# Optimization experiments

Hardware: AMD Instinct MI355X
Metric: run time of the kernel (lower is better)

## Reference

```python
import jax, jax.numpy as jnp
import numpy as np

BSZ, S, F, K, PI = 32, 4096, 512, 4, 1


def setup_inputs() -> dict:
    key = jax.random.key(0)
    ks = jax.random.split(key, 5)
    x = jax.random.normal(ks[0], (BSZ, S, F), dtype=jnp.float32)
    s = 1.0 / np.float32(np.sqrt(F))
    Wu = jax.random.normal(ks[1], (F, F), dtype=jnp.float32) * s
    P = jax.random.normal(ks[2], (F // K, F), dtype=jnp.float32) * s
    Q = jax.random.normal(ks[3], (F, PI * F), dtype=jnp.float32) * s
    Bb = jax.random.normal(ks[4], (F // K, PI * F), dtype=jnp.float32) * 0.01
    return {"x": x, "Wu": Wu, "P": P, "Q": Q, "Bb": Bb}


def reference(x, Wu, P, Q, Bb):
    # x: [B, S, F]
    B_, S_, F_ = x.shape
    Fk = P.shape[0]          # F // k
    k = F_ // Fk
    piF = Q.shape[1]
    # Ux = relu(x @ Wu): [B, S, F]
    Ux = jax.nn.relu(jnp.einsum('bsf,fg->bsg', x, Wu))
    # KMaxPooling over sequence axis: transpose to [B, F, S], top_k -> [B, F, k]
    topv = jax.lax.top_k(jnp.transpose(Ux, (0, 2, 1)), k)[0]
    # original does a raw reshape [B, F, k] -> [B, k, F] (element order preserved)
    z = topv.reshape(B_, k, F_)
    # P is reshaped in call() from [F/k, F] to [F, F/k]
    P2 = P.reshape(F_, Fk)
    # diag(z_i) @ P2 == z_i[:, None] * P2 -> [B, k, F, F/k], then per-i reshape to [B, F/k, F]
    zp = (z[:, :, :, None] * P2[None, None, :, :]).reshape(B_, k, Fk, F_)
    # @ Q, bias add, relu: [B, k, F/k, pi*F]
    out = jax.nn.relu(jnp.einsum('bkmf,fq->bkmq', zp, Q) + Bb[None, None, :, :])
    # concat over k along axis 1 -> [B, F, pi*F]
    return out.reshape(B_, F_, piF)
```

## Files before the change

### kernel.cpp

```cpp
#include <hip/hip_runtime.h>

#define BSZ   32
#define SEQ   4096
#define FDIM  512
#define KTOP  4
#define FK    128
#define MTOT  (BSZ * SEQ)
#define NCHUNK 32

#define BM2  256
#define BN2  256
#define BK2  64
#define NKT  (FDIM / BK2)

typedef __attribute__((ext_vector_type(8))) short bf16x8;
typedef __attribute__((ext_vector_type(4))) float f32x4;
typedef __attribute__((ext_vector_type(8))) unsigned short u16x8;

typedef __attribute__((address_space(1))) void void_g;
typedef __attribute__((address_space(3))) void void_l;

static __device__ __forceinline__ void load_lds16(const void* g, void* l) {
  __builtin_amdgcn_global_load_lds((void_g*)g, (void_l*)l, 16, 0, 0);
}

static __device__ __forceinline__ unsigned short f2bf(float f) {
  unsigned int u = __float_as_uint(f);
  unsigned int r = (u + 0x7fffu + ((u >> 16) & 1u)) >> 16;
  return (unsigned short)r;
}

static __device__ __forceinline__ void sort2(float& a, float& b) {
  float mx = fmaxf(a, b), mn = fminf(a, b); a = mx; b = mn;
}
static __device__ __forceinline__ void sort4(float& a, float& b, float& c, float& d) {
  sort2(a, b); sort2(c, d); sort2(a, c); sort2(b, d); sort2(b, c);
}
static __device__ __forceinline__ void merge4(float& a, float& b, float& c, float& d,
                                              float e, float f, float g, float h) {
  float m0 = fmaxf(a, h), m1 = fmaxf(b, g), m2 = fmaxf(c, f), m3 = fmaxf(d, e);
  sort2(m0, m2); sort2(m1, m3); sort2(m0, m1); sort2(m2, m3);
  a = m0; b = m1; c = m2; d = m3;
}

__global__ __launch_bounds__(256) void cvt_wuT_kernel(const float* __restrict__ Wu,
                                                      unsigned short* __restrict__ WuT) {
  int nn = blockIdx.x;
  for (int k = threadIdx.x; k < FDIM; k += blockDim.x)
    WuT[(size_t)nn * FDIM + k] = f2bf(Wu[(size_t)k * FDIM + nn]);
}

__global__ __launch_bounds__(256) void compute_R_kernel(const float* __restrict__ P,
                                                        const float* __restrict__ Q,
                                                        float* __restrict__ R) {
  int g = blockIdx.y;
  int q = blockIdx.x * 256 + threadIdx.x;
  __shared__ float p2[FK];
  if (threadIdx.x < FK) p2[threadIdx.x] = P[(size_t)g * FK + threadIdx.x];
  __syncthreads();
  const float* Qb = Q + (size_t)((g & 3) * FK) * FDIM + q;
  float s = 0.f;
#pragma unroll 8
  for (int m = 0; m < FK; ++m) s = fmaf(p2[m], Qb[(size_t)m * FDIM], s);
  R[(size_t)g * FDIM + q] = s;
}

__global__ __launch_bounds__(512, 1) void gemm_topk_kernel(
    const float* __restrict__ X, const unsigned short* __restrict__ Bt,
    float* __restrict__ cand) {
  __shared__ __align__(16) unsigned short As[2][BM2 * BK2];
  __shared__ __align__(16) unsigned short Bs[2][BM2 * BK2];

  const int tid = threadIdx.x;
  const int lane = tid & 63;
  const int w = tid >> 6;
  const int wm = w & 1, wn = w >> 1;

  const int xcd = blockIdx.x & 7;
  const int jj = blockIdx.x >> 3;
  const int t = xcd * 128 + jj;
  const int mtile = t >> 1, ntile = t & 1;
  const int m0 = mtile * BM2, n0 = ntile * BN2;

  const int arow = tid >> 3;
  const int asc = tid & 7;
  const int aswz = (arow & 7) << 4;
  const float* axp[4];
  int aldst[4];
#pragma unroll
  for (int i = 0; i < 4; ++i) {
    const int row = i * 64 + arow;
    axp[i] = X + (size_t)(m0 + row) * FDIM + asc * 8;
    aldst[i] = row * 128 + ((asc * 16) ^ aswz);
  }
  float4 arA[4][2];

#define ALOADS(kt)                                                             \
  {                                                                            \
    _Pragma("unroll") for (int i = 0; i < 4; ++i) {                            \
      const float4* p = (const float4*)(axp[i] + (kt) * BK2);                  \
      arA[i][0] = p[0];                                                        \
      arA[i][1] = p[1];                                                        \
    }                                                                          \
  }

#define AWRITES(buf)                                                           \
  {                                                                            \
    _Pragma("unroll") for (int i = 0; i < 4; ++i) {                            \
      u16x8 o;                                                                 \
      o[0] = f2bf(arA[i][0].x); o[1] = f2bf(arA[i][0].y);                      \
      o[2] = f2bf(arA[i][0].z); o[3] = f2bf(arA[i][0].w);                      \
      o[4] = f2bf(arA[i][1].x); o[5] = f2bf(arA[i][1].y);                      \
      o[6] = f2bf(arA[i][1].z); o[7] = f2bf(arA[i][1].w);                      \
      *(u16x8*)((char*)As[buf] + aldst[i]) = o;                                \
    }                                                                          \
  }

  const char* bsrc[4];
#pragma unroll
  for (int i = 0; i < 4; ++i) {
    int o = i * 8192 + tid * 16;
    int row = o >> 7;
    int colb = (o & 127) ^ ((row & 7) << 4);
    bsrc[i] = (const char*)(Bt + (size_t)(n0 + row) * FDIM) + colb;
  }
  const int ldst = (tid >> 6) * 512;

#define STAGE_B(kt, buf)                                                       \
  {                                                                            \
    _Pragma("unroll") for (int i = 0; i < 4; ++i)                              \
        load_lds16(bsrc[i] + (kt) * 128, (void*)(&Bs[buf][i * 4096 + ldst]));  \
  }

  const int lr = lane & 15;
  const int g16 = lane >> 4;
  const int swz = (lr & 7) << 4;
  const int arow0 = (wm * 128 + lr) * 128;
  const int brow0 = (wn * 64 + lr) * 128;

  f32x4 acc[8][4];
#pragma unroll
  for (int mi = 0; mi < 8; ++mi)
#pragma unroll
    for (int ni = 0; ni < 4; ++ni) acc[mi][ni] = {0.f, 0.f, 0.f, 0.f};

#define PHASE(Ap, Bp, mh, nh, ...)                                             \
  {                                                                            \
    bf16x8 af[4][2], bfr[2][2];                                                \
    _Pragma("unroll") for (int j = 0; j < 4; ++j)                              \
        _Pragma("unroll") for (int kq = 0; kq < 2; ++kq)                       \
            af[j][kq] = *(const bf16x8*)((Ap) + arow0 + ((mh)*4 + j) * 2048 +  \
                                         ((kq * 64 + g16 * 16) ^ swz));        \
    _Pragma("unroll") for (int j = 0; j < 2; ++j)                              \
        _Pragma("unroll") for (int kq = 0; kq < 2; ++kq)                       \
            bfr[j][kq] = *(const bf16x8*)((Bp) + brow0 + ((nh)*2 + j) * 2048 + \
                                          ((kq * 64 + g16 * 16) ^ swz));       \
    __VA_ARGS__;                                                               \
    __builtin_amdgcn_s_barrier();                                              \
    __builtin_amdgcn_s_setprio(1);                                             \
    _Pragma("unroll") for (int j = 0; j < 4; ++j)                              \
        _Pragma("unroll") for (int jn = 0; jn < 2; ++jn)                       \
            _Pragma("unroll") for (int kq = 0; kq < 2; ++kq)                   \
                acc[(mh)*4 + j][(nh)*2 + jn] =                                 \
                    __builtin_amdgcn_mfma_f32_16x16x32_bf16(                   \
                        af[j][kq], bfr[jn][kq], acc[(mh)*4 + j][(nh)*2 + jn],  \
                        0, 0, 0);                                              \
    __builtin_amdgcn_s_setprio(0);                                             \
  }

  ALOADS(0);
  AWRITES(0);
  STAGE_B(0, 0);
  asm volatile("s_waitcnt vmcnt(0) lgkmcnt(0)" ::: "memory");
  __builtin_amdgcn_s_barrier();
  __builtin_amdgcn_sched_barrier(0);

#pragma unroll 1
  for (int kt = 0; kt < NKT; ++kt) {
    const int c = kt & 1;
    const char* Ap = (const char*)As[c];
    const char* Bp = (const char*)Bs[c];
    const int last = (kt == NKT - 1);

    PHASE(Ap, Bp, 0, 0, if (!last) ALOADS(kt + 1));
    __builtin_amdgcn_s_barrier();
    PHASE(Ap, Bp, 0, 1, if (!last) STAGE_B(kt + 1, c ^ 1));
    __builtin_amdgcn_s_barrier();
    PHASE(Ap, Bp, 1, 0, );
    __builtin_amdgcn_s_barrier();
    PHASE(Ap, Bp, 1, 1, if (!last) AWRITES(c ^ 1));
    asm volatile("s_waitcnt vmcnt(0) lgkmcnt(0)" ::: "memory");
    __builtin_amdgcn_s_barrier();
    __builtin_amdgcn_sched_barrier(0);
  }

  const int mchunk = mtile * 2 + wm;
  const int b = mchunk >> 5;
  const int chunk = mchunk & 31;
#pragma unroll
  for (int ni = 0; ni < 4; ++ni) {
    float a0 = acc[0][ni][0], a1 = acc[0][ni][1], a2 = acc[0][ni][2], a3 = acc[0][ni][3];
    sort4(a0, a1, a2, a3);
#pragma unroll
    for (int mi = 1; mi < 8; ++mi) {
      float b0 = acc[mi][ni][0], b1 = acc[mi][ni][1];
      float b2 = acc[mi][ni][2], b3 = acc[mi][ni][3];
      sort4(b0, b1, b2, b3);
      merge4(a0, a1, a2, a3, b0, b1, b2, b3);
    }
#pragma unroll
    for (int off = 16; off < 64; off <<= 1) {
      float e0 = __shfl_xor(a0, off), e1 = __shfl_xor(a1, off);
      float e2 = __shfl_xor(a2, off), e3 = __shfl_xor(a3, off);
      merge4(a0, a1, a2, a3, e0, e1, e2, e3);
    }
    if (lane < 16) {
      const int f = n0 + wn * 64 + ni * 16 + lane;
      float4 v; v.x = a0; v.y = a1; v.z = a2; v.w = a3;
      *(float4*)(cand + (((size_t)(b * FDIM + f)) * NCHUNK + chunk) * 4) = v;
    }
  }
}

__global__ __launch_bounds__(256) void out_kernel(
    const float* __restrict__ cand, const float* __restrict__ R,
    const float* __restrict__ Bb, float* __restrict__ out) {
  const int row = blockIdx.x * 4 + (threadIdx.x >> 6);
  const int lane = threadIdx.x & 63;
  const int b = row >> 9, ff = row & 511;
  const int m2 = ff & 127;

  const float4 cv = *(const float4*)(cand +
      (((size_t)(b * FDIM + ff)) * NCHUNK + (lane & 31)) * 4);
  float t0 = cv.x, t1 = cv.y, t2 = cv.z, t3 = cv.w;
#pragma unroll
  for (int off = 1; off < 32; off <<= 1) {
    float e0 = __shfl_xor(t0, off), e1 = __shfl_xor(t1, off);
    float e2 = __shfl_xor(t2, off), e3 = __shfl_xor(t3, off);
    merge4(t0, t1, t2, t3, e0, e1, e2, e3);
  }
  t0 = fmaxf(t0, 0.f); t1 = fmaxf(t1, 0.f); t2 = fmaxf(t2, 0.f); t3 = fmaxf(t3, 0.f);

  const float* R0 = R + (size_t)(4 * m2) * FDIM;
  const float* Bbr = Bb + (size_t)m2 * FDIM;
  float* ob = out + (size_t)row * FDIM;
#pragma unroll
  for (int jq = 0; jq < 8; ++jq) {
    const int q = jq * 64 + lane;
    float s = Bbr[q];
    s = fmaf(t0, R0[q], s);
    s = fmaf(t1, R0[FDIM + q], s);
    s = fmaf(t2, R0[2 * FDIM + q], s);
    s = fmaf(t3, R0[3 * FDIM + q], s);
    ob[q] = s > 0.f ? s : 0.f;
  }
}

extern "C" void kernel_launch(void* const* d_in, const int* in_sizes, int n_in,
                              void* d_out, int out_size, void* d_ws, size_t ws_size,
                              hipStream_t stream) {
  const float* x  = (const float*)d_in[0];
  const float* Wu = (const float*)d_in[1];
  const float* P  = (const float*)d_in[2];
  const float* Q  = (const float*)d_in[3];
  const float* Bb = (const float*)d_in[4];
  float* out = (float*)d_out;

  char* ws = (char*)d_ws;
  unsigned short* wuT = (unsigned short*)(ws);
  float*          R   = (float*)(ws + 524288L);
  float*          cand= (float*)(ws + 1572864L);

  hipLaunchKernelGGL(cvt_wuT_kernel, dim3(512), dim3(256), 0, stream, Wu, wuT);
  hipLaunchKernelGGL(compute_R_kernel, dim3(2, 512), dim3(256), 0, stream, P, Q, R);
  hipLaunchKernelGGL(gemm_topk_kernel, dim3(1024), dim3(512), 0, stream, x, wuT, cand);
  hipLaunchKernelGGL(out_kernel, dim3(BSZ * FDIM / 4), dim3(256), 0, stream, cand, R, Bb, out);
}
```

Baseline: 151.0 us.

## Switch GEMM to 32x32x16 MFMA and prefetch A two k-steps ahead

Replaces the 16x16x32 bf16 MFMA tiling with 32x32x16 MFMAs, using f32x16 accumulators and two phases per k-tile instead of four. This reduces LDS fragment reads per MFMA and the number of barriers. Global A loads are now issued two iterations ahead and waited on with a partial vmcnt, so load latency overlaps more compute. The top-k epilogue is reworked for the 32x32 output layout and needs only one cross-lane shuffle merge. The risks are higher register pressure and possible LDS bank conflicts with the new swizzle indexing.

```diff
diff --git a/kernel.cpp b/kernel.cpp
--- a/kernel.cpp
+++ b/kernel.cpp
@@ -15,6 +15,7 @@
 
 typedef __attribute__((ext_vector_type(8))) short bf16x8;
 typedef __attribute__((ext_vector_type(4))) float f32x4;
+typedef __attribute__((ext_vector_type(16))) float f32x16;
 typedef __attribute__((ext_vector_type(8))) unsigned short u16x8;
 
 typedef __attribute__((address_space(1))) void void_g;
@@ -132,48 +133,51 @@
         load_lds16(bsrc[i] + (kt) * 128, (void*)(&Bs[buf][i * 4096 + ldst]));  \
   }
 
-  const int lr = lane & 15;
-  const int g16 = lane >> 4;
-  const int swz = (lr & 7) << 4;
-  const int arow0 = (wm * 128 + lr) * 128;
-  const int brow0 = (wn * 64 + lr) * 128;
-
-  f32x4 acc[8][4];
-#pragma unroll
-  for (int mi = 0; mi < 8; ++mi)
-#pragma unroll
-    for (int ni = 0; ni < 4; ++ni) acc[mi][ni] = {0.f, 0.f, 0.f, 0.f};
-
-#define PHASE(Ap, Bp, mh, nh, ...)                                             \
+  const int l32 = lane & 31;
+  const int g32 = lane >> 5;
+  const int swz = (lane & 7) << 4;
+  const int arow0 = (wm * 128 + l32) * 128;
+  const int brow0 = (wn * 64 + l32) * 128;
+
+  f32x16 acc[4][2];
+#pragma unroll
+  for (int mi = 0; mi < 4; ++mi)
+#pragma unroll
+    for (int ni = 0; ni < 2; ++ni) acc[mi][ni] = (f32x16)(0.0f);
+
+#define PHASE2(Ap, Bp, p, ...)                                                 \
   {                                                                            \
     bf16x8 af[4][2], bfr[2][2];                                                \
-    _Pragma("unroll") for (int j = 0; j < 4; ++j)                              \
-        _Pragma("unroll") for (int kq = 0; kq < 2; ++kq)                       \
-            af[j][kq] = *(const bf16x8*)((Ap) + arow0 + ((mh)*4 + j) * 2048 +  \
-                                         ((kq * 64 + g16 * 16) ^ swz));        \
-    _Pragma("unroll") for (int j = 0; j < 2; ++j)                              \
-        _Pragma("unroll") for (int kq = 0; kq < 2; ++kq)                       \
-            bfr[j][kq] = *(const bf16x8*)((Bp) + brow0 + ((nh)*2 + j) * 2048 + \
-                                          ((kq * 64 + g16 * 16) ^ swz));       \
+    _Pragma("unroll") for (int mi = 0; mi < 4; ++mi)                           \
+        _Pragma("unroll") for (int q = 0; q < 2; ++q)                          \
+            af[mi][q] = *(const bf16x8*)((Ap) + arow0 + mi * 4096 +            \
+                (((2 * (p) + q) * 32 + g32 * 16) ^ swz));                      \
+    _Pragma("unroll") for (int ni = 0; ni < 2; ++ni)                           \
+        _Pragma("unroll") for (int q = 0; q < 2; ++q)                          \
+            bfr[ni][q] = *(const bf16x8*)((Bp) + brow0 + ni * 4096 +           \
+                (((2 * (p) + q) * 32 + g32 * 16) ^ swz));                      \
     __VA_ARGS__;                                                               \
     __builtin_amdgcn_s_barrier();                                              \
     __builtin_amdgcn_s_setprio(1);                                             \
-    _Pragma("unroll") for (int j = 0; j < 4; ++j)                              \
-        _Pragma("unroll") for (int jn = 0; jn < 2; ++jn)                       \
-            _Pragma("unroll") for (int kq = 0; kq < 2; ++kq)                   \
-                acc[(mh)*4 + j][(nh)*2 + jn] =                                 \
-                    __builtin_amdgcn_mfma_f32_16x16x32_bf16(                   \
-                        af[j][kq], bfr[jn][kq], acc[(mh)*4 + j][(nh)*2 + jn],  \
-                        0, 0, 0);                                              \
+    _Pragma("unroll") for (int mi = 0; mi < 4; ++mi)                           \
+        _Pragma("unroll") for (int ni = 0; ni < 2; ++ni)                       \
+            _Pragma("unroll") for (int q = 0; q < 2; ++q)                      \
+                acc[mi][ni] = __builtin_amdgcn_mfma_f32_32x32x16_bf16(         \
+                    af[mi][q], bfr[ni][q], acc[mi][ni], 0, 0, 0);              \
     __builtin_amdgcn_s_setprio(0);                                             \
   }
+
+#define WAIT_BAR(n)                                                            \
+  asm volatile("s_waitcnt vmcnt(" #n ") lgkmcnt(0)" ::: "memory");             \
+  __builtin_amdgcn_s_barrier();                                                \
+  __builtin_amdgcn_sched_barrier(0);
 
   ALOADS(0);
   AWRITES(0);
   STAGE_B(0, 0);
-  asm volatile("s_waitcnt vmcnt(0) lgkmcnt(0)" ::: "memory");
-  __builtin_amdgcn_s_barrier();
+  ALOADS(1);
   __builtin_amdgcn_sched_barrier(0);
+  WAIT_BAR(8);
 
 #pragma unroll 1
   for (int kt = 0; kt < NKT; ++kt) {
@@ -182,40 +186,43 @@
     const char* Bp = (const char*)Bs[c];
     const int last = (kt == NKT - 1);
 
-    PHASE(Ap, Bp, 0, 0, if (!last) ALOADS(kt + 1));
+    PHASE2(Ap, Bp, 0, if (!last) STAGE_B(kt + 1, c ^ 1));
     __builtin_amdgcn_s_barrier();
-    PHASE(Ap, Bp, 0, 1, if (!last) STAGE_B(kt + 1, c ^ 1));
-    __builtin_amdgcn_s_barrier();
-    PHASE(Ap, Bp, 1, 0, );
-    __builtin_amdgcn_s_barrier();
-    PHASE(Ap, Bp, 1, 1, if (!last) AWRITES(c ^ 1));
-    asm volatile("s_waitcnt vmcnt(0) lgkmcnt(0)" ::: "memory");
-    __builtin_amdgcn_s_barrier();
-    __builtin_amdgcn_sched_barrier(0);
+    PHASE2(Ap, Bp, 1,
+           if (!last) {
+             AWRITES(c ^ 1);
+             if (kt + 2 < NKT) ALOADS(kt + 2);
+           });
+    if (kt + 2 < NKT) { WAIT_BAR(8); } else { WAIT_BAR(0); }
   }
 
   const int mchunk = mtile * 2 + wm;
   const int b = mchunk >> 5;
   const int chunk = mchunk & 31;
 #pragma unroll
-  for (int ni = 0; ni < 4; ++ni) {
-    float a0 = acc[0][ni][0], a1 = acc[0][ni][1], a2 = acc[0][ni][2], a3 = acc[0][ni][3];
-    sort4(a0, a1, a2, a3);
-#pragma unroll
-    for (int mi = 1; mi < 8; ++mi) {
-      float b0 = acc[mi][ni][0], b1 = acc[mi][ni][1];
-      float b2 = acc[mi][ni][2], b3 = acc[mi][ni][3];
-      sort4(b0, b1, b2, b3);
-      merge4(a0, a1, a2, a3, b0, b1, b2, b3);
+  for (int ni = 0; ni < 2; ++ni) {
+    float a0, a1, a2, a3;
+    {
+      a0 = acc[0][ni][0]; a1 = acc[0][ni][1]; a2 = acc[0][ni][2]; a3 = acc[0][ni][3];
+      sort4(a0, a1, a2, a3);
     }
 #pragma unroll
-    for (int off = 16; off < 64; off <<= 1) {
-      float e0 = __shfl_xor(a0, off), e1 = __shfl_xor(a1, off);
-      float e2 = __shfl_xor(a2, off), e3 = __shfl_xor(a3, off);
+    for (int mi = 0; mi < 4; ++mi)
+#pragma unroll
+      for (int gq = 0; gq < 4; ++gq) {
+        if (mi == 0 && gq == 0) continue;
+        float b0 = acc[mi][ni][gq * 4 + 0], b1 = acc[mi][ni][gq * 4 + 1];
+        float b2 = acc[mi][ni][gq * 4 + 2], b3 = acc[mi][ni][gq * 4 + 3];
+        sort4(b0, b1, b2, b3);
+        merge4(a0, a1, a2, a3, b0, b1, b2, b3);
+      }
+    {
+      float e0 = __shfl_xor(a0, 32), e1 = __shfl_xor(a1, 32);
+      float e2 = __shfl_xor(a2, 32), e3 = __shfl_xor(a3, 32);
       merge4(a0, a1, a2, a3, e0, e1, e2, e3);
     }
-    if (lane < 16) {
-      const int f = n0 + wn * 64 + ni * 16 + lane;
+    if (lane < 32) {
+      const int f = n0 + wn * 64 + ni * 32 + l32;
       float4 v; v.x = a0; v.y = a1; v.z = a2; v.w = a3;
       *(float4*)(cand + (((size_t)(b * FDIM + f)) * NCHUNK + chunk) * 4) = v;
     }
```

Measured after the change: 140.4 us. 7.0% less time.
